# Optimization experiments

Measured on AMD Instinct MI355X. Metric: run time of the kernel, lower is better.

## Reference

```python
import jax, jax.numpy as jnp
import numpy as np

N, NFEAT, NHID, NH2, NCLASS = 16384, 512, 256, 64, 10


def setup_inputs() -> dict:
    key = jax.random.key(0)
    ks = jax.random.split(key, 12)
    x = jax.random.normal(ks[0], (N, NFEAT), dtype=jnp.float32)
    # dense (row-normalized-style) adjacency; sparsified to ~avg degree 32
    a = jax.random.uniform(ks[1], (N, N), dtype=jnp.float32)
    mask = (jax.random.uniform(ks[2], (N, N)) < (32.0 / N)).astype(jnp.float32)
    adj = a * mask / 32.0
    s = lambda fin: 1.0 / np.sqrt(fin)
    W1 = jax.random.uniform(ks[3], (NFEAT, NHID), jnp.float32, -s(NFEAT), s(NFEAT))
    b1 = jax.random.uniform(ks[4], (NHID,), jnp.float32, -s(NFEAT), s(NFEAT))
    W2 = jax.random.uniform(ks[5], (NHID, NH2), jnp.float32, -s(NHID), s(NHID))
    b2 = jax.random.uniform(ks[6], (NH2,), jnp.float32, -s(NHID), s(NHID))
    W3 = jax.random.uniform(ks[7], (NH2, 32), jnp.float32, -s(NH2), s(NH2))
    b3 = jax.random.uniform(ks[8], (32,), jnp.float32, -s(NH2), s(NH2))
    W4 = jax.random.uniform(ks[9], (32, 16), jnp.float32, -s(32), s(32))
    b4 = jax.random.uniform(ks[10], (16,), jnp.float32, -s(32), s(32))
    W5 = jax.random.uniform(ks[11], (16, NCLASS), jnp.float32, -s(16), s(16))
    b5 = jnp.zeros((NCLASS,), jnp.float32)
    return {"x": x, "adj": adj, "W1": W1, "b1": b1, "W2": W2, "b2": b2,
            "W3": W3, "b3": b3, "W4": W4, "b4": b4, "W5": W5, "b5": b5}


def reference(x, adj, W1, b1, W2, b2, W3, b3, W4, b4, W5, b5):
    # GraphConvolution: adj @ (x @ W) + b
    h = jax.nn.relu(adj @ (x @ W1) + b1)          # [N, NHID]
    h = adj @ (h @ W2) + b2                        # [N, 64]
    g = jnp.max(h, axis=0)                         # [64] graph max-pool
    g = jax.nn.relu(g @ W3 + b3)                   # [32]
    g = jax.nn.relu(g @ W4 + b4)                   # [16]
    return g @ W5 + b5                             # [NCLASS]
```

## Files before the change

kernel.cpp:

```cpp
#include <hip/hip_runtime.h>
#include <hip/hip_bf16.h>
#include <cstdint>

#define NROW 16384
#define NFEAT 512
#define NHID 256
#define NH2 64
#define CAP 96

#define BM 128
#define BN 64
#define BK 16
#define GEMM_BLOCKS 512

__global__ __launch_bounds__(256, 4) void k0_csr_gemm(
    const float* __restrict__ X, const float* __restrict__ W1,
    const float* __restrict__ adj,
    float* __restrict__ XW1, float* __restrict__ vals,
    int* __restrict__ cols, int* __restrict__ cnt) {
  __shared__ float As[BK][BM + 4];
  __shared__ float Bs[BK][BN];
  const int t = threadIdx.x;

  if (blockIdx.x < GEMM_BLOCKS) {
    const int bm = (blockIdx.x >> 2) * BM;
    const int bn = (blockIdx.x & 3) * BN;
    const int tx = t & 15;
    const int ty = t >> 4;
    const int ar = t >> 1;
    const int ak = (t & 1) * 8;
    const int bk = t >> 4;
    const int bnn = (t & 15) * 4;
    float acc[8][4] = {};
    for (int k0 = 0; k0 < NFEAT; k0 += BK) {
      const float4 a0 = *(const float4*)&X[(size_t)(bm + ar) * NFEAT + k0 + ak];
      const float4 a1 = *(const float4*)&X[(size_t)(bm + ar) * NFEAT + k0 + ak + 4];
      const float4 b0 = *(const float4*)&W1[(size_t)(k0 + bk) * NHID + bn + bnn];
      As[ak + 0][ar] = a0.x; As[ak + 1][ar] = a0.y;
      As[ak + 2][ar] = a0.z; As[ak + 3][ar] = a0.w;
      As[ak + 4][ar] = a1.x; As[ak + 5][ar] = a1.y;
      As[ak + 6][ar] = a1.z; As[ak + 7][ar] = a1.w;
      *(float4*)&Bs[bk][bnn] = b0;
      __syncthreads();
#pragma unroll
      for (int k = 0; k < BK; ++k) {
        float a[8], b[4];
#pragma unroll
        for (int i = 0; i < 8; ++i) a[i] = As[k][ty * 8 + i];
#pragma unroll
        for (int j = 0; j < 4; ++j) b[j] = Bs[k][tx * 4 + j];
#pragma unroll
        for (int i = 0; i < 8; ++i)
#pragma unroll
          for (int j = 0; j < 4; ++j) acc[i][j] += a[i] * b[j];
      }
      __syncthreads();
    }
#pragma unroll
    for (int i = 0; i < 8; ++i) {
      float4 v = {acc[i][0], acc[i][1], acc[i][2], acc[i][3]};
      *(float4*)&XW1[(size_t)(bm + ty * 8 + i) * NHID + bn + tx * 4] = v;
    }
  } else {
    const int wave = t >> 6;
    const int lane = t & 63;
    const int row = (blockIdx.x - GEMM_BLOCKS) * 4 + wave;
    const float* arow = adj + (size_t)row * NROW;
    int count = 0;
    for (int c0 = 0; c0 < NROW; c0 += 256) {
      const float4 v = *(const float4*)&arow[c0 + lane * 4];
#pragma unroll
      for (int k = 0; k < 4; ++k) {
        const float val = (k == 0) ? v.x : (k == 1) ? v.y : (k == 2) ? v.z : v.w;
        const unsigned long long m = __ballot(val != 0.0f);
        if (val != 0.0f) {
          const int pos = count + __popcll(m & ((1ull << lane) - 1ull));
          if (pos < CAP) {
            vals[(size_t)row * CAP + pos] = val;
            cols[(size_t)row * CAP + pos] = c0 + lane * 4 + k;
          }
        }
        count += __popcll(m);
      }
    }
    if (lane == 0) cnt[row] = count < CAP ? count : CAP;
  }
}

__global__ __launch_bounds__(256, 4) void k1_prop1(
    const float* __restrict__ XW1, const float* __restrict__ vals,
    const int* __restrict__ cols, const int* __restrict__ cnt,
    const float* __restrict__ b1, const float* __restrict__ W2,
    float* __restrict__ H1W2) {
  __shared__ int   scl[4][CAP];
  __shared__ float sv[4][CAP];
  __shared__ float sh[4][NHID];
  __shared__ float sp[4][256];
  const int t = threadIdx.x;
  const int row0 = blockIdx.x * 4;
  {
    const int r = t >> 6, j = t & 63;
    const int n = cnt[row0 + r];
    for (int jj = j; jj < n; jj += 64) {
      scl[r][jj] = cols[(size_t)(row0 + r) * CAP + jj];
      sv[r][jj]  = vals[(size_t)(row0 + r) * CAP + jj];
    }
  }
  __syncthreads();
  const float bias = b1[t];
  for (int r = 0; r < 4; ++r) {
    const int n = cnt[row0 + r];
    float a0 = 0.f, a1 = 0.f, a2 = 0.f, a3 = 0.f;
    int k = 0;
    for (; k + 4 <= n; k += 4) {
      a0 += sv[r][k + 0] * XW1[(size_t)scl[r][k + 0] * NHID + t];
      a1 += sv[r][k + 1] * XW1[(size_t)scl[r][k + 1] * NHID + t];
      a2 += sv[r][k + 2] * XW1[(size_t)scl[r][k + 2] * NHID + t];
      a3 += sv[r][k + 3] * XW1[(size_t)scl[r][k + 3] * NHID + t];
    }
    for (; k < n; ++k) a0 += sv[r][k] * XW1[(size_t)scl[r][k] * NHID + t];
    const float h = a0 + a1 + a2 + a3 + bias;
    sh[r][t] = h > 0.f ? h : 0.f;
  }
  __syncthreads();
  const int c = t & 63, q = t >> 6;
  float p0 = 0.f, p1 = 0.f, p2 = 0.f, p3 = 0.f;
#pragma unroll 8
  for (int kk = 0; kk < 64; ++kk) {
    const int kidx = q * 64 + kk;
    const float w = W2[kidx * NH2 + c];
    p0 += sh[0][kidx] * w;
    p1 += sh[1][kidx] * w;
    p2 += sh[2][kidx] * w;
    p3 += sh[3][kidx] * w;
  }
  sp[0][t] = p0; sp[1][t] = p1; sp[2][t] = p2; sp[3][t] = p3;
  __syncthreads();
  {
    const int r2 = t >> 6, c2 = t & 63;
    H1W2[(size_t)(row0 + r2) * NH2 + c2] =
        sp[r2][c2] + sp[r2][c2 + 64] + sp[r2][c2 + 128] + sp[r2][c2 + 192];
  }
}

__global__ __launch_bounds__(256, 4) void k2_prop2(
    const float* __restrict__ H1W2, const float* __restrict__ vals,
    const int* __restrict__ cols, const int* __restrict__ cnt,
    const float* __restrict__ b2, float* __restrict__ blockmax) {
  __shared__ int   scl[4][CAP];
  __shared__ float sv[4][CAP];
  __shared__ float smax[4][NH2];
  const int t = threadIdx.x;
  const int w = t >> 6, l = t & 63;
  const int row = blockIdx.x * 4 + w;
  const int n = cnt[row];
  for (int jj = l; jj < n; jj += 64) {
    scl[w][jj] = cols[(size_t)row * CAP + jj];
    sv[w][jj]  = vals[(size_t)row * CAP + jj];
  }
  __syncthreads();
  float a0 = 0.f, a1 = 0.f, a2 = 0.f, a3 = 0.f;
  int k = 0;
  for (; k + 4 <= n; k += 4) {
    a0 += sv[w][k + 0] * H1W2[(size_t)scl[w][k + 0] * NH2 + l];
    a1 += sv[w][k + 1] * H1W2[(size_t)scl[w][k + 1] * NH2 + l];
    a2 += sv[w][k + 2] * H1W2[(size_t)scl[w][k + 2] * NH2 + l];
    a3 += sv[w][k + 3] * H1W2[(size_t)scl[w][k + 3] * NH2 + l];
  }
  for (; k < n; ++k) a0 += sv[w][k] * H1W2[(size_t)scl[w][k] * NH2 + l];
  smax[w][l] = a0 + a1 + a2 + a3 + b2[l];
  __syncthreads();
  if (t < NH2) {
    const float m = fmaxf(fmaxf(smax[0][t], smax[1][t]),
                          fmaxf(smax[2][t], smax[3][t]));
    blockmax[(size_t)blockIdx.x * NH2 + t] = m;
  }
}

__global__ __launch_bounds__(256) void k3_colmax(const float* __restrict__ blockmax,
                                                 float* __restrict__ partial) {
  __shared__ float sm[256];
  const int t = threadIdx.x, c = t & 63, q = t >> 6;
  const int base = blockIdx.x * 64;
  float m = -3.4e38f;
  for (int r = q; r < 64; r += 4)
    m = fmaxf(m, blockmax[(size_t)(base + r) * NH2 + c]);
  sm[t] = m;
  __syncthreads();
  if (t < 64)
    partial[blockIdx.x * 64 + t] =
        fmaxf(fmaxf(sm[t], sm[t + 64]), fmaxf(sm[t + 128], sm[t + 192]));
}

__global__ __launch_bounds__(64) void k4_final(const float* __restrict__ partial,
                                               const float* __restrict__ W3,
                                               const float* __restrict__ b3,
                                               const float* __restrict__ W4,
                                               const float* __restrict__ b4,
                                               const float* __restrict__ W5,
                                               const float* __restrict__ b5,
                                               float* __restrict__ out) {
  __shared__ float g[64], t3[32], t4[16];
  const int t = threadIdx.x;
  float m = -3.4e38f;
  for (int p = 0; p < 64; ++p) m = fmaxf(m, partial[p * 64 + t]);
  g[t] = m;
  __syncthreads();
  if (t < 32) {
    float acc = b3[t];
    for (int k = 0; k < 64; ++k) acc += g[k] * W3[k * 32 + t];
    t3[t] = acc > 0.f ? acc : 0.f;
  }
  __syncthreads();
  if (t < 16) {
    float acc = b4[t];
    for (int k = 0; k < 32; ++k) acc += t3[k] * W4[k * 16 + t];
    t4[t] = acc > 0.f ? acc : 0.f;
  }
  __syncthreads();
  if (t < 10) {
    float acc = b5[t];
    for (int k = 0; k < 16; ++k) acc += t4[k] * W5[k * 10 + t];
    out[t] = acc;
  }
}

extern "C" void kernel_launch(void* const* d_in, const int* in_sizes, int n_in,
                              void* d_out, int out_size, void* d_ws, size_t ws_size,
                              hipStream_t stream) {
  const float* x   = (const float*)d_in[0];
  const float* adj = (const float*)d_in[1];
  const float* W1  = (const float*)d_in[2];
  const float* b1  = (const float*)d_in[3];
  const float* W2  = (const float*)d_in[4];
  const float* b2  = (const float*)d_in[5];
  const float* W3  = (const float*)d_in[6];
  const float* b3  = (const float*)d_in[7];
  const float* W4  = (const float*)d_in[8];
  const float* b4  = (const float*)d_in[9];
  const float* W5  = (const float*)d_in[10];
  const float* b5  = (const float*)d_in[11];
  float* out = (float*)d_out;

  char* ws = (char*)d_ws;
  float* XW1      = (float*)(ws);
  float* vals     = (float*)(ws + (size_t)16 * 1024 * 1024);
  int*   cols     = (int*)  (ws + (size_t)24 * 1024 * 1024);
  int*   cnt      = (int*)  (ws + (size_t)32 * 1024 * 1024);
  float* H1W2     = (float*)(ws + (size_t)36 * 1024 * 1024);
  float* blockmax = (float*)(ws + (size_t)40 * 1024 * 1024);
  float* partial  = (float*)(ws + (size_t)44 * 1024 * 1024);

  k0_csr_gemm<<<GEMM_BLOCKS + NROW / 4, 256, 0, stream>>>(x, W1, adj, XW1, vals, cols, cnt);
  k1_prop1<<<NROW / 4, 256, 0, stream>>>(XW1, vals, cols, cnt, b1, W2, H1W2);
  k2_prop2<<<NROW / 4, 256, 0, stream>>>(H1W2, vals, cols, cnt, b2, blockmax);
  k3_colmax<<<64, 256, 0, stream>>>(blockmax, partial);
  k4_final<<<1, 64, 0, stream>>>(partial, W3, b3, W4, b4, W5, b5, out);
}
```

Before: 1.499 ms.

## Fuse adjacency CSR extraction into first propagation kernel with prefetched nontemporal loads

Moves the dense-adjacency scan out of the combined GEMM kernel and into the first propagation kernel, so each wave compacts its row into shared memory and uses it directly without a round trip through global CSR arrays. The adjacency stream now uses nontemporal loads with a one-step software prefetch, and the XW1 gather is widened to float4 per lane with one wave per row instead of the whole block looping over rows. The GEMM no longer overlaps with the adjacency scan inside one launch, so the scan now runs after the GEMM completes.

After: 1.491 ms. About the same (-0.6%).

```diff
diff --git a/kernel.cpp b/kernel.cpp
--- a/kernel.cpp
+++ b/kernel.cpp
@@ -8,131 +8,135 @@
 #define NH2 64
 #define CAP 96
 
+typedef float vfloat4 __attribute__((ext_vector_type(4)));
+
 #define BM 128
 #define BN 64
 #define BK 16
-#define GEMM_BLOCKS 512
-
-__global__ __launch_bounds__(256, 4) void k0_csr_gemm(
+
+__global__ __launch_bounds__(256, 4) void kA_gemm(
     const float* __restrict__ X, const float* __restrict__ W1,
-    const float* __restrict__ adj,
-    float* __restrict__ XW1, float* __restrict__ vals,
-    int* __restrict__ cols, int* __restrict__ cnt) {
+    float* __restrict__ XW1) {
   __shared__ float As[BK][BM + 4];
   __shared__ float Bs[BK][BN];
   const int t = threadIdx.x;
-
-  if (blockIdx.x < GEMM_BLOCKS) {
-    const int bm = (blockIdx.x >> 2) * BM;
-    const int bn = (blockIdx.x & 3) * BN;
-    const int tx = t & 15;
-    const int ty = t >> 4;
-    const int ar = t >> 1;
-    const int ak = (t & 1) * 8;
-    const int bk = t >> 4;
-    const int bnn = (t & 15) * 4;
-    float acc[8][4] = {};
-    for (int k0 = 0; k0 < NFEAT; k0 += BK) {
-      const float4 a0 = *(const float4*)&X[(size_t)(bm + ar) * NFEAT + k0 + ak];
-      const float4 a1 = *(const float4*)&X[(size_t)(bm + ar) * NFEAT + k0 + ak + 4];
-      const float4 b0 = *(const float4*)&W1[(size_t)(k0 + bk) * NHID + bn + bnn];
-      As[ak + 0][ar] = a0.x; As[ak + 1][ar] = a0.y;
-      As[ak + 2][ar] = a0.z; As[ak + 3][ar] = a0.w;
-      As[ak + 4][ar] = a1.x; As[ak + 5][ar] = a1.y;
-      As[ak + 6][ar] = a1.z; As[ak + 7][ar] = a1.w;
-      *(float4*)&Bs[bk][bnn] = b0;
-      __syncthreads();
-#pragma unroll
-      for (int k = 0; k < BK; ++k) {
-        float a[8], b[4];
-#pragma unroll
-        for (int i = 0; i < 8; ++i) a[i] = As[k][ty * 8 + i];
-#pragma unroll
-        for (int j = 0; j < 4; ++j) b[j] = Bs[k][tx * 4 + j];
-#pragma unroll
-        for (int i = 0; i < 8; ++i)
-#pragma unroll
-          for (int j = 0; j < 4; ++j) acc[i][j] += a[i] * b[j];
-      }
-      __syncthreads();
+  const int bm = (blockIdx.x >> 2) * BM;
+  const int bn = (blockIdx.x & 3) * BN;
+  const int tx = t & 15;
+  const int ty = t >> 4;
+  const int ar = t >> 1;
+  const int ak = (t & 1) * 8;
+  const int bk = t >> 4;
+  const int bnn = (t & 15) * 4;
+  float acc[8][4] = {};
+  for (int k0 = 0; k0 < NFEAT; k0 += BK) {
+    const float4 a0 = *(const float4*)&X[(size_t)(bm + ar) * NFEAT + k0 + ak];
+    const float4 a1 = *(const float4*)&X[(size_t)(bm + ar) * NFEAT + k0 + ak + 4];
+    const float4 b0 = *(const float4*)&W1[(size_t)(k0 + bk) * NHID + bn + bnn];
+    As[ak + 0][ar] = a0.x; As[ak + 1][ar] = a0.y;
+    As[ak + 2][ar] = a0.z; As[ak + 3][ar] = a0.w;
+    As[ak + 4][ar] = a1.x; As[ak + 5][ar] = a1.y;
+    As[ak + 6][ar] = a1.z; As[ak + 7][ar] = a1.w;
+    *(float4*)&Bs[bk][bnn] = b0;
+    __syncthreads();
+#pragma unroll
+    for (int k = 0; k < BK; ++k) {
+      float a[8], b[4];
+#pragma unroll
+      for (int i = 0; i < 8; ++i) a[i] = As[k][ty * 8 + i];
+#pragma unroll
+      for (int j = 0; j < 4; ++j) b[j] = Bs[k][tx * 4 + j];
+#pragma unroll
+      for (int i = 0; i < 8; ++i)
+#pragma unroll
+        for (int j = 0; j < 4; ++j) acc[i][j] += a[i] * b[j];
     }
-#pragma unroll
-    for (int i = 0; i < 8; ++i) {
-      float4 v = {acc[i][0], acc[i][1], acc[i][2], acc[i][3]};
-      *(float4*)&XW1[(size_t)(bm + ty * 8 + i) * NHID + bn + tx * 4] = v;
-    }
-  } else {
-    const int wave = t >> 6;
-    const int lane = t & 63;
-    const int row = (blockIdx.x - GEMM_BLOCKS) * 4 + wave;
-    const float* arow = adj + (size_t)row * NROW;
-    int count = 0;
-    for (int c0 = 0; c0 < NROW; c0 += 256) {
-      const float4 v = *(const float4*)&arow[c0 + lane * 4];
-#pragma unroll
-      for (int k = 0; k < 4; ++k) {
-        const float val = (k == 0) ? v.x : (k == 1) ? v.y : (k == 2) ? v.z : v.w;
-        const unsigned long long m = __ballot(val != 0.0f);
-        if (val != 0.0f) {
-          const int pos = count + __popcll(m & ((1ull << lane) - 1ull));
-          if (pos < CAP) {
-            vals[(size_t)row * CAP + pos] = val;
-            cols[(size_t)row * CAP + pos] = c0 + lane * 4 + k;
-          }
-        }
-        count += __popcll(m);
-      }
-    }
-    if (lane == 0) cnt[row] = count < CAP ? count : CAP;
-  }
-}
-
-__global__ __launch_bounds__(256, 4) void k1_prop1(
-    const float* __restrict__ XW1, const float* __restrict__ vals,
-    const int* __restrict__ cols, const int* __restrict__ cnt,
+    __syncthreads();
+  }
+#pragma unroll
+  for (int i = 0; i < 8; ++i) {
+    float4 v = {acc[i][0], acc[i][1], acc[i][2], acc[i][3]};
+    *(float4*)&XW1[(size_t)(bm + ty * 8 + i) * NHID + bn + tx * 4] = v;
+  }
+}
+
+__global__ __launch_bounds__(256, 4) void kB_stream_prop1(
+    const float* __restrict__ adj, const float* __restrict__ XW1,
     const float* __restrict__ b1, const float* __restrict__ W2,
+    float* __restrict__ vals, int* __restrict__ cols, int* __restrict__ cnt,
     float* __restrict__ H1W2) {
   __shared__ int   scl[4][CAP];
   __shared__ float sv[4][CAP];
   __shared__ float sh[4][NHID];
   __shared__ float sp[4][256];
   const int t = threadIdx.x;
+  const int w = t >> 6, lane = t & 63;
   const int row0 = blockIdx.x * 4;
-  {
-    const int r = t >> 6, j = t & 63;
-    const int n = cnt[row0 + r];
-    for (int jj = j; jj < n; jj += 64) {
-      scl[r][jj] = cols[(size_t)(row0 + r) * CAP + jj];
-      sv[r][jj]  = vals[(size_t)(row0 + r) * CAP + jj];
+  const int row = row0 + w;
+
+  const float* arow = adj + (size_t)row * NROW;
+  int count = 0;
+  vfloat4 nxt = __builtin_nontemporal_load((const vfloat4*)&arow[lane * 4]);
+  for (int c0 = 0; c0 < NROW; c0 += 256) {
+    const vfloat4 v = nxt;
+    if (c0 + 256 < NROW)
+      nxt = __builtin_nontemporal_load((const vfloat4*)&arow[c0 + 256 + lane * 4]);
+#pragma unroll
+    for (int k = 0; k < 4; ++k) {
+      const float val = v[k];
+      const unsigned long long m = __ballot(val != 0.0f);
+      if (val != 0.0f) {
+        const int pos = count + __popcll(m & ((1ull << lane) - 1ull));
+        if (pos < CAP) { sv[w][pos] = val; scl[w][pos] = c0 + lane * 4 + k; }
+      }
+      count += __popcll(m);
     }
   }
-  __syncthreads();
-  const float bias = b1[t];
-  for (int r = 0; r < 4; ++r) {
-    const int n = cnt[row0 + r];
-    float a0 = 0.f, a1 = 0.f, a2 = 0.f, a3 = 0.f;
-    int k = 0;
-    for (; k + 4 <= n; k += 4) {
-      a0 += sv[r][k + 0] * XW1[(size_t)scl[r][k + 0] * NHID + t];
-      a1 += sv[r][k + 1] * XW1[(size_t)scl[r][k + 1] * NHID + t];
-      a2 += sv[r][k + 2] * XW1[(size_t)scl[r][k + 2] * NHID + t];
-      a3 += sv[r][k + 3] * XW1[(size_t)scl[r][k + 3] * NHID + t];
-    }
-    for (; k < n; ++k) a0 += sv[r][k] * XW1[(size_t)scl[r][k] * NHID + t];
-    const float h = a0 + a1 + a2 + a3 + bias;
-    sh[r][t] = h > 0.f ? h : 0.f;
-  }
-  __syncthreads();
+  const int n = count < CAP ? count : CAP;
+  if (lane == 0) cnt[row] = n;
+  for (int j = lane; j < n; j += 64) {
+    cols[(size_t)row * CAP + j] = scl[w][j];
+    vals[(size_t)row * CAP + j] = sv[w][j];
+  }
+
+  float4 a0 = {0,0,0,0}, a1 = {0,0,0,0}, a2 = {0,0,0,0}, a3 = {0,0,0,0};
+  int k = 0;
+  for (; k + 4 <= n; k += 4) {
+    const float v0 = sv[w][k], v1 = sv[w][k+1], v2 = sv[w][k+2], v3 = sv[w][k+3];
+    const int   c0i = scl[w][k], c1i = scl[w][k+1], c2i = scl[w][k+2], c3i = scl[w][k+3];
+    const float4 x0 = *(const float4*)&XW1[(size_t)c0i * NHID + lane * 4];
+    const float4 x1 = *(const float4*)&XW1[(size_t)c1i * NHID + lane * 4];
+    const float4 x2 = *(const float4*)&XW1[(size_t)c2i * NHID + lane * 4];
+    const float4 x3 = *(const float4*)&XW1[(size_t)c3i * NHID + lane * 4];
+    a0.x += v0*x0.x; a0.y += v0*x0.y; a0.z += v0*x0.z; a0.w += v0*x0.w;
+    a1.x += v1*x1.x; a1.y += v1*x1.y; a1.z += v1*x1.z; a1.w += v1*x1.w;
+    a2.x += v2*x2.x; a2.y += v2*x2.y; a2.z += v2*x2.z; a2.w += v2*x2.w;
+    a3.x += v3*x3.x; a3.y += v3*x3.y; a3.z += v3*x3.z; a3.w += v3*x3.w;
+  }
+  for (; k < n; ++k) {
+    const float v0 = sv[w][k];
+    const float4 x0 = *(const float4*)&XW1[(size_t)scl[w][k] * NHID + lane * 4];
+    a0.x += v0*x0.x; a0.y += v0*x0.y; a0.z += v0*x0.z; a0.w += v0*x0.w;
+  }
+  const float4 bb = *(const float4*)&b1[lane * 4];
+  float4 h;
+  h.x = fmaxf(a0.x + a1.x + a2.x + a3.x + bb.x, 0.f);
+  h.y = fmaxf(a0.y + a1.y + a2.y + a3.y + bb.y, 0.f);
+  h.z = fmaxf(a0.z + a1.z + a2.z + a3.z + bb.z, 0.f);
+  h.w = fmaxf(a0.w + a1.w + a2.w + a3.w + bb.w, 0.f);
+  *(float4*)&sh[w][lane * 4] = h;
+  __syncthreads();
+
   const int c = t & 63, q = t >> 6;
   float p0 = 0.f, p1 = 0.f, p2 = 0.f, p3 = 0.f;
 #pragma unroll 8
   for (int kk = 0; kk < 64; ++kk) {
     const int kidx = q * 64 + kk;
-    const float w = W2[kidx * NH2 + c];
-    p0 += sh[0][kidx] * w;
-    p1 += sh[1][kidx] * w;
-    p2 += sh[2][kidx] * w;
-    p3 += sh[3][kidx] * w;
+    const float wv = W2[kidx * NH2 + c];
+    p0 += sh[0][kidx] * wv;
+    p1 += sh[1][kidx] * wv;
+    p2 += sh[2][kidx] * wv;
+    p3 += sh[3][kidx] * wv;
   }
   sp[0][t] = p0; sp[1][t] = p1; sp[2][t] = p2; sp[3][t] = p3;
   __syncthreads();
@@ -143,7 +147,7 @@
   }
 }
 
-__global__ __launch_bounds__(256, 4) void k2_prop2(
+__global__ __launch_bounds__(256, 4) void kC_prop2(
     const float* __restrict__ H1W2, const float* __restrict__ vals,
     const int* __restrict__ cols, const int* __restrict__ cnt,
     const float* __restrict__ b2, float* __restrict__ blockmax) {
@@ -177,8 +181,8 @@
   }
 }
 
-__global__ __launch_bounds__(256) void k3_colmax(const float* __restrict__ blockmax,
-                                                 float* __restrict__ partial) {
+__global__ __launch_bounds__(256) void kD1_colmax(const float* __restrict__ blockmax,
+                                                  float* __restrict__ partial) {
   __shared__ float sm[256];
   const int t = threadIdx.x, c = t & 63, q = t >> 6;
   const int base = blockIdx.x * 64;
@@ -192,14 +196,14 @@
         fmaxf(fmaxf(sm[t], sm[t + 64]), fmaxf(sm[t + 128], sm[t + 192]));
 }
 
-__global__ __launch_bounds__(64) void k4_final(const float* __restrict__ partial,
-                                               const float* __restrict__ W3,
-                                               const float* __restrict__ b3,
-                                               const float* __restrict__ W4,
-                                               const float* __restrict__ b4,
-                                               const float* __restrict__ W5,
-                                               const float* __restrict__ b5,
-                                               float* __restrict__ out) {
+__global__ __launch_bounds__(64) void kD2_final(const float* __restrict__ partial,
+                                                const float* __restrict__ W3,
+                                                const float* __restrict__ b3,
+                                                const float* __restrict__ W4,
+                                                const float* __restrict__ b4,
+                                                const float* __restrict__ W5,
+                                                const float* __restrict__ b5,
+                                                float* __restrict__ out) {
   __shared__ float g[64], t3[32], t4[16];
   const int t = threadIdx.x;
   float m = -3.4e38f;
@@ -251,9 +255,10 @@
   float* blockmax = (float*)(ws + (size_t)40 * 1024 * 1024);
   float* partial  = (float*)(ws + (size_t)44 * 1024 * 1024);
 
-  k0_csr_gemm<<<GEMM_BLOCKS + NROW / 4, 256, 0, stream>>>(x, W1, adj, XW1, vals, cols, cnt);
-  k1_prop1<<<NROW / 4, 256, 0, stream>>>(XW1, vals, cols, cnt, b1, W2, H1W2);
-  k2_prop2<<<NROW / 4, 256, 0, stream>>>(H1W2, vals, cols, cnt, b2, blockmax);
-  k3_colmax<<<64, 256, 0, stream>>>(blockmax, partial);
-  k4_final<<<1, 64, 0, stream>>>(partial, W3, b3, W4, b4, W5, b5, out);
-}
+  kA_gemm<<<512, 256, 0, stream>>>(x, W1, XW1);
+  kB_stream_prop1<<<NROW / 4, 256, 0, stream>>>(adj, XW1, b1, W2,
+                                                vals, cols, cnt, H1W2);
+  kC_prop2<<<NROW / 4, 256, 0, stream>>>(H1W2, vals, cols, cnt, b2, blockmax);
+  kD1_colmax<<<64, 256, 0, stream>>>(blockmax, partial);
+  kD2_final<<<1, 64, 0, stream>>>(partial, W3, b3, W4, b4, W5, b5, out);
+}
```
